# Kernel optimization log

Hardware: AMD Instinct MI355X
Metric: run time of the kernel (lower is better)

The kernel has to match this reference:

```python
import jax, jax.numpy as jnp
import numpy as np

NUM_CODES = 8192
CODE_DEPTH = 64
D_MODEL = 1024
NUM_LEVELS = 1


def setup_inputs() -> dict:
    key = jax.random.key(0)
    k1, k2, k3, k4 = jax.random.split(key, 4)
    x = jax.random.normal(k1, (8, 2048, D_MODEL), dtype=jnp.float32)
    # nn.Linear(d_model, code_depth): weight [code_depth, d_model], bias [code_depth]
    W_down = jax.random.normal(k2, (CODE_DEPTH, D_MODEL), dtype=jnp.float32) * 0.02
    b_down = jnp.zeros((CODE_DEPTH,), dtype=jnp.float32)
    # codebook = torch.randn(num_levels, num_codes, code_depth)
    codebook = jax.random.normal(k3, (NUM_LEVELS, NUM_CODES, CODE_DEPTH), dtype=jnp.float32)
    return {"x": x, "W_down": W_down, "b_down": b_down, "codebook": codebook}


def reference(x, W_down, b_down, codebook):
    # downsample: Linear(d_model -> code_depth), level 0
    soft = jnp.einsum("bsd,cd->bsc", x, W_down) + b_down  # [B,S,C]
    book = codebook[0]  # [K,C]
    # cdist(x, book).argmin == argmin of squared distances (sqrt is monotone)
    x2 = jnp.sum(soft * soft, axis=-1, keepdims=True)      # [B,S,1]
    c2 = jnp.sum(book * book, axis=-1)                     # [K]
    xc = jnp.einsum("bsc,kc->bsk", soft, book)             # [B,S,K]
    sq_dist = x2 - 2.0 * xc + c2                           # [B,S,K]
    code_indices = jnp.argmin(sq_dist, axis=-1)            # [B,S] int
    hard = book[code_indices]                              # [B,S,C]
    # training-mode losses (mse_loss = mean over all elements)
    commitment_loss = jnp.mean((jax.lax.stop_gradient(hard) - soft) ** 2)
    embedding_loss = jnp.mean((hard - jax.lax.stop_gradient(soft)) ** 2)
    # straight-through estimator
    hard_ste = soft + jax.lax.stop_gradient(hard - soft)
    return (soft, code_indices, hard_ste, commitment_loss, embedding_loss)
```

## Files before the change

kernel.cpp:

```cpp
#include <hip/hip_runtime.h>

#define M_TOT   16384
#define DM      1024
#define CD      64
#define NCODES  8192
#define NCHUNK  16
#define CPC     (NCODES / NCHUNK)
#define CTILE   16

#define SOFT_OFF  0
#define IDX_OFF   1048576
#define HARD_OFF  1064960
#define LOSS_OFF  2113536

__global__ __launch_bounds__(256) void compute_c2(const float* __restrict__ book,
                                                  float* __restrict__ c2) {
    const int k = blockIdx.x * 256 + threadIdx.x;
    const float4* p = (const float4*)(book + (size_t)k * CD);
    float s = 0.0f;
#pragma unroll
    for (int q = 0; q < CD / 4; ++q) {
        const float4 v = p[q];
        s = fmaf(v.x, v.x, s);
        s = fmaf(v.y, v.y, s);
        s = fmaf(v.z, v.z, s);
        s = fmaf(v.w, v.w, s);
    }
    c2[k] = s;
}

__global__ __launch_bounds__(1024, 1) void soft_fused(const float* __restrict__ x,
                                                      const float* __restrict__ W,
                                                      const float* __restrict__ bias,
                                                      float* __restrict__ out_soft) {
    __shared__ float smem[8704];
    float (*xt)[16][68] = (float (*)[16][68])smem;
    float (*wt)[16][68] = (float (*)[16][68])(smem + 4352);
    float (*pb)[32][65] = (float (*)[32][65])smem;

    const int tid = threadIdx.x;
    const int kg  = tid >> 8;
    const int t   = tid & 255;
    const int r0  = blockIdx.x * 64;
    const int rg  = t >> 4;
    const int cg  = t & 15;

    float acc[4][4] = {};

    for (int k0 = kg * 256; k0 < kg * 256 + 256; k0 += 16) {
        {
            const int row = t >> 2;
            const int kq  = (t & 3) * 4;
            const float4 v = *(const float4*)(x + (size_t)(r0 + row) * DM + k0 + kq);
            xt[kg][kq + 0][row] = v.x; xt[kg][kq + 1][row] = v.y;
            xt[kg][kq + 2][row] = v.z; xt[kg][kq + 3][row] = v.w;
            const float4 w = *(const float4*)(W + (size_t)row * DM + k0 + kq);
            wt[kg][kq + 0][row] = w.x; wt[kg][kq + 1][row] = w.y;
            wt[kg][kq + 2][row] = w.z; wt[kg][kq + 3][row] = w.w;
        }
        __syncthreads();
#pragma unroll
        for (int kk = 0; kk < 16; ++kk) {
            const float4 xv = *(const float4*)&xt[kg][kk][rg * 4];
            const float4 wv = *(const float4*)&wt[kg][kk][cg * 4];
            const float xa[4] = {xv.x, xv.y, xv.z, xv.w};
            const float wa[4] = {wv.x, wv.y, wv.z, wv.w};
#pragma unroll
            for (int r = 0; r < 4; ++r)
#pragma unroll
                for (int q = 0; q < 4; ++q)
                    acc[r][q] = fmaf(xa[r], wa[q], acc[r][q]);
        }
        __syncthreads();
    }

#pragma unroll
    for (int half = 0; half < 2; ++half) {
        if ((rg >> 3) == half) {
#pragma unroll
            for (int r = 0; r < 4; ++r)
                *(float4*)&pb[kg][(rg & 7) * 4 + r][cg * 4] =
                    make_float4(acc[r][0], acc[r][1], acc[r][2], acc[r][3]);
        }
        __syncthreads();
        if (tid < 512) {
            const int row = tid >> 4;
            const int qd  = tid & 15;
            float4 s = *(const float4*)&pb[0][row][qd * 4];
#pragma unroll
            for (int g = 1; g < 4; ++g) {
                const float4 v = *(const float4*)&pb[g][row][qd * 4];
                s.x += v.x; s.y += v.y; s.z += v.z; s.w += v.w;
            }
            const float4 bb = *(const float4*)(bias + qd * 4);
            s.x += bb.x; s.y += bb.y; s.z += bb.z; s.w += bb.w;
            *(float4*)(out_soft + (size_t)(r0 + half * 32 + row) * CD + qd * 4) = s;
        }
        __syncthreads();
    }
}

__global__ __launch_bounds__(256, 4) void dist_argmin3(const float* __restrict__ soft,
                                                       const float* __restrict__ book,
                                                       const float* __restrict__ c2,
                                                       float* __restrict__ cand_d,
                                                       int* __restrict__ cand_i) {
    const int row   = blockIdx.x * 256 + threadIdx.x;
    const int kbase = blockIdx.y * CPC;
    const float4* sp = (const float4*)(soft + (size_t)row * CD);

    float mind = 3.4e38f;
    int   mini = kbase;

    for (int kt = 0; kt < CPC; kt += CTILE) {
        const float4* bp = (const float4*)(book + (size_t)(kbase + kt) * CD);
        float acc[CTILE] = {};
#pragma unroll
        for (int q = 0; q < 16; ++q) {
            const float4 sv = sp[q];
#pragma unroll
            for (int c = 0; c < CTILE; ++c) {
                const float4 bv = bp[(size_t)c * 16 + q];
                acc[c] = fmaf(sv.x, bv.x, acc[c]);
                acc[c] = fmaf(sv.y, bv.y, acc[c]);
                acc[c] = fmaf(sv.z, bv.z, acc[c]);
                acc[c] = fmaf(sv.w, bv.w, acc[c]);
            }
        }
        const int kk0 = kbase + kt;
#pragma unroll
        for (int c = 0; c < CTILE; ++c) {
            const float dd = fmaf(-2.f, acc[c], c2[kk0 + c]);
            if (dd < mind) { mind = dd; mini = kk0 + c; }
        }
    }

    cand_d[blockIdx.y * M_TOT + row] = mind;
    cand_i[blockIdx.y * M_TOT + row] = mini;
}

__global__ __launch_bounds__(256) void finalize(const float* __restrict__ book,
                                                const float* __restrict__ cand_d,
                                                const int* __restrict__ cand_i,
                                                float* __restrict__ out) {
    __shared__ float rd[256];
    __shared__ int   ri[256];
    __shared__ int   ksels[16];
    __shared__ float red[256];

    const int tid  = threadIdx.x;
    const int rloc = tid >> 4;
    const int g    = tid & 15;
    const int row  = blockIdx.x * 16 + rloc;

    rd[tid] = cand_d[(size_t)g * M_TOT + row];
    ri[tid] = cand_i[(size_t)g * M_TOT + row];
    __syncthreads();

    if (g == 0) {
        float bd = rd[rloc * 16];
        int   bi = ri[rloc * 16];
#pragma unroll
        for (int j = 1; j < 16; ++j) {
            const float dd = rd[rloc * 16 + j];
            if (dd < bd) { bd = dd; bi = ri[rloc * 16 + j]; }
        }
        ksels[rloc] = bi;
        out[IDX_OFF + row] = (float)bi;
    }
    __syncthreads();

    const int k  = ksels[rloc];
    const int dq = g * 4;

    const float4 h = *(const float4*)(book + (size_t)k * CD + dq);
    const float4 s = *(const float4*)(out + SOFT_OFF + (size_t)row * CD + dq);

    const float dx = h.x - s.x, dy = h.y - s.y, dz = h.z - s.z, dw = h.w - s.w;
    float4 ste;
    ste.x = s.x + dx; ste.y = s.y + dy; ste.z = s.z + dz; ste.w = s.w + dw;
    *(float4*)(out + HARD_OFF + (size_t)row * CD + dq) = ste;

    red[tid] = dx * dx + dy * dy + dz * dz + dw * dw;
    __syncthreads();
#pragma unroll
    for (int sh = 128; sh > 0; sh >>= 1) {
        if (tid < sh) red[tid] += red[tid + sh];
        __syncthreads();
    }
    if (tid == 0) {
        const float v = red[0] * (1.0f / (float)(M_TOT * CD));
        atomicAdd(out + LOSS_OFF, v);
        atomicAdd(out + LOSS_OFF + 1, v);
    }
}

extern "C" void kernel_launch(void* const* d_in, const int* in_sizes, int n_in,
                              void* d_out, int out_size, void* d_ws, size_t ws_size,
                              hipStream_t stream) {
    const float* x    = (const float*)d_in[0];
    const float* W    = (const float*)d_in[1];
    const float* bias = (const float*)d_in[2];
    const float* book = (const float*)d_in[3];
    float* out = (float*)d_out;

    float* ws     = (float*)d_ws;
    float* c2     = ws;
    float* cand_d = ws + NCODES;
    int*   cand_i = (int*)(cand_d + NCHUNK * M_TOT);

    compute_c2<<<NCODES / 256, 256, 0, stream>>>(book, c2);
    soft_fused<<<M_TOT / 64, 1024, 0, stream>>>(x, W, bias, out + SOFT_OFF);
    dist_argmin3<<<dim3(M_TOT / 256, NCHUNK), 256, 0, stream>>>(out + SOFT_OFF, book, c2,
                                                                cand_d, cand_i);
    hipMemsetAsync(out + LOSS_OFF, 0, 2 * sizeof(float), stream);
    finalize<<<M_TOT / 16, 256, 0, stream>>>(book, cand_d, cand_i, out);
}
```

Measured before the change: 563.6 us.

## Use bf16 MFMA two-pass distance search with fp32 rescoring of near candidates

Replaces the fp32 scalar distance/argmin kernel with a bf16 MFMA pipeline. A first pass finds each row's approximate minimum distance. A second pass collects every (row, code) pair within a fixed margin of that minimum, and an fp32 rescore picks the exact argmin by 64-bit atomicMin. This moves the dominant 16384x8192x64 GEMM onto matrix cores, at the cost of running the GEMM twice, extra conversion kernels, and atomics. The candidate list is capped and the margin is fixed, so an overflow or a bf16 error larger than the margin could change the selected indices.

```diff
diff --git a/kernel.cpp b/kernel.cpp
--- a/kernel.cpp
+++ b/kernel.cpp
@@ -1,4 +1,5 @@
 #include <hip/hip_runtime.h>
+#include <hip/hip_bf16.h>
 
 #define M_TOT   16384
 #define DM      1024
@@ -7,11 +8,27 @@
 #define NCHUNK  16
 #define CPC     (NCODES / NCHUNK)
 #define CTILE   16
+#define CSPLIT  8
+#define CODES_PER_CHUNK (NCODES / CSPLIT)
+#define DELTA   2.0f
+#define CAP     (1u << 19)
 
 #define SOFT_OFF  0
 #define IDX_OFF   1048576
 #define HARD_OFF  1064960
 #define LOSS_OFF  2113536
+
+typedef __attribute__((ext_vector_type(8)))  short bfrag;
+typedef __attribute__((ext_vector_type(16))) float f32x16;
+
+__device__ __forceinline__ unsigned mapf(float d) {
+    unsigned u = __float_as_uint(d);
+    return (u & 0x80000000u) ? ~u : (u | 0x80000000u);
+}
+__device__ __forceinline__ float unmapf(unsigned m) {
+    unsigned u = (m & 0x80000000u) ? (m ^ 0x80000000u) : ~m;
+    return __uint_as_float(u);
+}
 
 __global__ __launch_bounds__(256) void compute_c2(const float* __restrict__ book,
                                                   float* __restrict__ c2) {
@@ -21,12 +38,25 @@
 #pragma unroll
     for (int q = 0; q < CD / 4; ++q) {
         const float4 v = p[q];
-        s = fmaf(v.x, v.x, s);
-        s = fmaf(v.y, v.y, s);
-        s = fmaf(v.z, v.z, s);
-        s = fmaf(v.w, v.w, s);
+        s = fmaf(v.x, v.x, s); s = fmaf(v.y, v.y, s);
+        s = fmaf(v.z, v.z, s); s = fmaf(v.w, v.w, s);
     }
     c2[k] = s;
+}
+
+__global__ __launch_bounds__(256) void cvt_bf16(const float* __restrict__ src,
+                                                unsigned short* __restrict__ dst,
+                                                int n4) {
+    const int i = blockIdx.x * 256 + threadIdx.x;
+    if (i >= n4) return;
+    const float4 v = ((const float4*)src)[i];
+    ushort4 o;
+    __hip_bfloat16 a;
+    a = __float2bfloat16(v.x); o.x = *(unsigned short*)&a;
+    a = __float2bfloat16(v.y); o.y = *(unsigned short*)&a;
+    a = __float2bfloat16(v.z); o.z = *(unsigned short*)&a;
+    a = __float2bfloat16(v.w); o.w = *(unsigned short*)&a;
+    ((ushort4*)dst)[i] = o;
 }
 
 __global__ __launch_bounds__(1024, 1) void soft_fused(const float* __restrict__ x,
@@ -100,6 +130,163 @@
     }
 }
 
+template<int PASS>
+__global__ __launch_bounds__(256, 4) void mfma_dist(const unsigned short* __restrict__ sbf,
+                                                    const unsigned short* __restrict__ bbf,
+                                                    const float* __restrict__ c2,
+                                                    unsigned* __restrict__ rowmin_u,
+                                                    unsigned* __restrict__ cnt,
+                                                    unsigned* __restrict__ list) {
+    const int tid  = threadIdx.x;
+    const int lane = tid & 63;
+    const int w    = tid >> 6;
+    const int cl   = lane & 31;
+    const int h    = lane >> 5;
+    const int r0w  = blockIdx.x * 128 + w * 32;
+    const int kbase = blockIdx.y * CODES_PER_CHUNK;
+
+    const unsigned short* sp = sbf + (size_t)(r0w + cl) * CD + 8 * h;
+    const bfrag a0 = *(const bfrag*)(sp + 0);
+    const bfrag a1 = *(const bfrag*)(sp + 16);
+    const bfrag a2 = *(const bfrag*)(sp + 32);
+    const bfrag a3 = *(const bfrag*)(sp + 48);
+
+    float rmin[16];
+    float thr[16];
+    if (PASS == 1) {
+#pragma unroll
+        for (int r = 0; r < 16; ++r) rmin[r] = 3.4e38f;
+    } else {
+#pragma unroll
+        for (int r = 0; r < 16; ++r)
+            thr[r] = unmapf(rowmin_u[r0w + (r & 3) + 8 * (r >> 2) + 4 * h]) + DELTA;
+    }
+
+#pragma unroll 2
+    for (int ct = 0; ct < CODES_PER_CHUNK / 32; ++ct) {
+        const int code = kbase + ct * 32 + cl;
+        const unsigned short* bp = bbf + (size_t)code * CD + 8 * h;
+        const bfrag b0 = *(const bfrag*)(bp + 0);
+        const bfrag b1 = *(const bfrag*)(bp + 16);
+        const bfrag b2 = *(const bfrag*)(bp + 32);
+        const bfrag b3 = *(const bfrag*)(bp + 48);
+
+        f32x16 acc;
+#pragma unroll
+        for (int r = 0; r < 16; ++r) acc[r] = 0.0f;
+        acc = __builtin_amdgcn_mfma_f32_32x32x16_bf16(a0, b0, acc, 0, 0, 0);
+        acc = __builtin_amdgcn_mfma_f32_32x32x16_bf16(a1, b1, acc, 0, 0, 0);
+        acc = __builtin_amdgcn_mfma_f32_32x32x16_bf16(a2, b2, acc, 0, 0, 0);
+        acc = __builtin_amdgcn_mfma_f32_32x32x16_bf16(a3, b3, acc, 0, 0, 0);
+
+        const float cc = c2[code];
+        if (PASS == 1) {
+#pragma unroll
+            for (int r = 0; r < 16; ++r)
+                rmin[r] = fminf(rmin[r], fmaf(-2.0f, acc[r], cc));
+        } else {
+            float hitmin = 1.0e30f;
+#pragma unroll
+            for (int r = 0; r < 16; ++r)
+                hitmin = fminf(hitmin, fmaf(-2.0f, acc[r], cc) - thr[r]);
+            if (hitmin < 0.0f) {
+#pragma unroll
+                for (int r = 0; r < 16; ++r) {
+                    const float dist = fmaf(-2.0f, acc[r], cc);
+                    if (dist < thr[r]) {
+                        const unsigned row = r0w + (r & 3) + 8 * (r >> 2) + 4 * h;
+                        const unsigned idx = atomicAdd(cnt, 1u);
+                        if (idx < CAP) list[idx] = (row << 13) | (unsigned)code;
+                    }
+                }
+            }
+        }
+    }
+
+    if (PASS == 1) {
+#pragma unroll
+        for (int r = 0; r < 16; ++r) {
+            float v = rmin[r];
+#pragma unroll
+            for (int m = 1; m <= 16; m <<= 1)
+                v = fminf(v, __shfl_xor(v, m, 64));
+            rmin[r] = v;
+        }
+        if (cl == 0) {
+#pragma unroll
+            for (int r = 0; r < 16; ++r)
+                atomicMin(&rowmin_u[r0w + (r & 3) + 8 * (r >> 2) + 4 * h], mapf(rmin[r]));
+        }
+    }
+}
+
+__global__ __launch_bounds__(256) void rescore(const float* __restrict__ soft,
+                                               const float* __restrict__ book,
+                                               const float* __restrict__ c2,
+                                               const unsigned* __restrict__ cnt,
+                                               const unsigned* __restrict__ list,
+                                               unsigned long long* __restrict__ rowkey) {
+    unsigned n = cnt[0];
+    if (n > CAP) n = CAP;
+    const unsigned i = blockIdx.x * 256 + threadIdx.x;
+    if (i >= n) return;
+    const unsigned pr = list[i];
+    const int row  = pr >> 13;
+    const int code = pr & 8191;
+    const float4* sp = (const float4*)(soft + (size_t)row * CD);
+    const float4* bp = (const float4*)(book + (size_t)code * CD);
+    float a = 0.0f;
+#pragma unroll
+    for (int q = 0; q < 16; ++q) {
+        const float4 s = sp[q], b = bp[q];
+        a = fmaf(s.x, b.x, a); a = fmaf(s.y, b.y, a);
+        a = fmaf(s.z, b.z, a); a = fmaf(s.w, b.w, a);
+    }
+    const float dist = fmaf(-2.0f, a, c2[code]);
+    const unsigned long long key = ((unsigned long long)mapf(dist) << 32) | (unsigned)code;
+    atomicMin(&rowkey[row], key);
+}
+
+__global__ __launch_bounds__(256) void finalize2(const float* __restrict__ book,
+                                                 const unsigned long long* __restrict__ rowkey,
+                                                 float* __restrict__ out) {
+    __shared__ int   ksels[16];
+    __shared__ float red[256];
+    const int tid  = threadIdx.x;
+    const int rloc = tid >> 4;
+    const int g    = tid & 15;
+    const int row  = blockIdx.x * 16 + rloc;
+
+    if (g == 0) {
+        const int k = (int)(unsigned)(rowkey[row] & 0xFFFFFFFFull);
+        ksels[rloc] = k;
+        out[IDX_OFF + row] = (float)k;
+    }
+    __syncthreads();
+
+    const int k  = ksels[rloc];
+    const int dq = g * 4;
+    const float4 h = *(const float4*)(book + (size_t)k * CD + dq);
+    const float4 s = *(const float4*)(out + SOFT_OFF + (size_t)row * CD + dq);
+    const float dx = h.x - s.x, dy = h.y - s.y, dz = h.z - s.z, dw = h.w - s.w;
+    float4 ste;
+    ste.x = s.x + dx; ste.y = s.y + dy; ste.z = s.z + dz; ste.w = s.w + dw;
+    *(float4*)(out + HARD_OFF + (size_t)row * CD + dq) = ste;
+
+    red[tid] = dx * dx + dy * dy + dz * dz + dw * dw;
+    __syncthreads();
+#pragma unroll
+    for (int sh = 128; sh > 0; sh >>= 1) {
+        if (tid < sh) red[tid] += red[tid + sh];
+        __syncthreads();
+    }
+    if (tid == 0) {
+        const float v = red[0] * (1.0f / (float)(M_TOT * CD));
+        atomicAdd(out + LOSS_OFF, v);
+        atomicAdd(out + LOSS_OFF + 1, v);
+    }
+}
+
 __global__ __launch_bounds__(256, 4) void dist_argmin3(const float* __restrict__ soft,
                                                        const float* __restrict__ book,
                                                        const float* __restrict__ c2,
@@ -108,10 +295,8 @@
     const int row   = blockIdx.x * 256 + threadIdx.x;
     const int kbase = blockIdx.y * CPC;
     const float4* sp = (const float4*)(soft + (size_t)row * CD);
-
     float mind = 3.4e38f;
     int   mini = kbase;
-
     for (int kt = 0; kt < CPC; kt += CTILE) {
         const float4* bp = (const float4*)(book + (size_t)(kbase + kt) * CD);
         float acc[CTILE] = {};
@@ -121,10 +306,8 @@
 #pragma unroll
             for (int c = 0; c < CTILE; ++c) {
                 const float4 bv = bp[(size_t)c * 16 + q];
-                acc[c] = fmaf(sv.x, bv.x, acc[c]);
-                acc[c] = fmaf(sv.y, bv.y, acc[c]);
-                acc[c] = fmaf(sv.z, bv.z, acc[c]);
-                acc[c] = fmaf(sv.w, bv.w, acc[c]);
+                acc[c] = fmaf(sv.x, bv.x, acc[c]); acc[c] = fmaf(sv.y, bv.y, acc[c]);
+                acc[c] = fmaf(sv.z, bv.z, acc[c]); acc[c] = fmaf(sv.w, bv.w, acc[c]);
             }
         }
         const int kk0 = kbase + kt;
@@ -134,29 +317,25 @@
             if (dd < mind) { mind = dd; mini = kk0 + c; }
         }
     }
-
     cand_d[blockIdx.y * M_TOT + row] = mind;
     cand_i[blockIdx.y * M_TOT + row] = mini;
 }
 
-__global__ __launch_bounds__(256) void finalize(const float* __restrict__ book,
-                                                const float* __restrict__ cand_d,
-                                                const int* __restrict__ cand_i,
-                                                float* __restrict__ out) {
+__global__ __launch_bounds__(256) void finalize_fb(const float* __restrict__ book,
+                                                   const float* __restrict__ cand_d,
+                                                   const int* __restrict__ cand_i,
+                                                   float* __restrict__ out) {
     __shared__ float rd[256];
     __shared__ int   ri[256];
     __shared__ int   ksels[16];
     __shared__ float red[256];
-
     const int tid  = threadIdx.x;
     const int rloc = tid >> 4;
     const int g    = tid & 15;
     const int row  = blockIdx.x * 16 + rloc;
-
     rd[tid] = cand_d[(size_t)g * M_TOT + row];
     ri[tid] = cand_i[(size_t)g * M_TOT + row];
     __syncthreads();
-
     if (g == 0) {
         float bd = rd[rloc * 16];
         int   bi = ri[rloc * 16];
@@ -169,18 +348,14 @@
         out[IDX_OFF + row] = (float)bi;
     }
     __syncthreads();
-
     const int k  = ksels[rloc];
     const int dq = g * 4;
-
     const float4 h = *(const float4*)(book + (size_t)k * CD + dq);
     const float4 s = *(const float4*)(out + SOFT_OFF + (size_t)row * CD + dq);
-
     const float dx = h.x - s.x, dy = h.y - s.y, dz = h.z - s.z, dw = h.w - s.w;
     float4 ste;
     ste.x = s.x + dx; ste.y = s.y + dy; ste.z = s.z + dz; ste.w = s.w + dw;
     *(float4*)(out + HARD_OFF + (size_t)row * CD + dq) = ste;
-
     red[tid] = dx * dx + dy * dy + dz * dz + dw * dw;
     __syncthreads();
 #pragma unroll
@@ -203,16 +378,44 @@
     const float* bias = (const float*)d_in[2];
     const float* book = (const float*)d_in[3];
     float* out = (float*)d_out;
-
-    float* ws     = (float*)d_ws;
-    float* c2     = ws;
-    float* cand_d = ws + NCODES;
-    int*   cand_i = (int*)(cand_d + NCHUNK * M_TOT);
-
-    compute_c2<<<NCODES / 256, 256, 0, stream>>>(book, c2);
-    soft_fused<<<M_TOT / 64, 1024, 0, stream>>>(x, W, bias, out + SOFT_OFF);
-    dist_argmin3<<<dim3(M_TOT / 256, NCHUNK), 256, 0, stream>>>(out + SOFT_OFF, book, c2,
-                                                                cand_d, cand_i);
+    char* ws = (char*)d_ws;
+
+    unsigned long long* rowkey = (unsigned long long*)(ws);
+    float*    c2       = (float*)(ws + 131072);
+    unsigned* rowmin_u = (unsigned*)(ws + 163840);
+    unsigned* cnt      = (unsigned*)(ws + 229376);
+    unsigned short* soft_bf = (unsigned short*)(ws + 229632);
+    unsigned short* book_bf = (unsigned short*)(ws + 2326784);
+    unsigned* list     = (unsigned*)(ws + 3375360);
+    const size_t NEED  = 5472512;
+
     hipMemsetAsync(out + LOSS_OFF, 0, 2 * sizeof(float), stream);
-    finalize<<<M_TOT / 16, 256, 0, stream>>>(book, cand_d, cand_i, out);
-}
+
+    if (ws_size >= NEED) {
+        compute_c2<<<NCODES / 256, 256, 0, stream>>>(book, c2);
+        cvt_bf16<<<(NCODES * CD / 4 + 255) / 256, 256, 0, stream>>>(book, book_bf,
+                                                                    NCODES * CD / 4);
+        soft_fused<<<M_TOT / 64, 1024, 0, stream>>>(x, W, bias, out + SOFT_OFF);
+        cvt_bf16<<<(M_TOT * CD / 4 + 255) / 256, 256, 0, stream>>>(out + SOFT_OFF, soft_bf,
+                                                                   M_TOT * CD / 4);
+        hipMemsetAsync(rowmin_u, 0xFF, M_TOT * sizeof(unsigned), stream);
+        hipMemsetAsync(rowkey, 0xFF, M_TOT * sizeof(unsigned long long), stream);
+        hipMemsetAsync(cnt, 0, 16, stream);
+
+        mfma_dist<1><<<dim3(M_TOT / 128, CSPLIT), 256, 0, stream>>>(soft_bf, book_bf, c2,
+                                                                    rowmin_u, cnt, list);
+        mfma_dist<2><<<dim3(M_TOT / 128, CSPLIT), 256, 0, stream>>>(soft_bf, book_bf, c2,
+                                                                    rowmin_u, cnt, list);
+        rescore<<<CAP / 256, 256, 0, stream>>>(out + SOFT_OFF, book, c2, cnt, list, rowkey);
+        finalize2<<<M_TOT / 16, 256, 0, stream>>>(book, rowkey, out);
+    } else {
+        float* c2f    = (float*)ws;
+        float* cand_d = c2f + NCODES;
+        int*   cand_i = (int*)(cand_d + NCHUNK * M_TOT);
+        compute_c2<<<NCODES / 256, 256, 0, stream>>>(book, c2f);
+        soft_fused<<<M_TOT / 64, 1024, 0, stream>>>(x, W, bias, out + SOFT_OFF);
+        dist_argmin3<<<dim3(M_TOT / 256, NCHUNK), 256, 0, stream>>>(out + SOFT_OFF, book,
+                                                                    c2f, cand_d, cand_i);
+        finalize_fb<<<M_TOT / 16, 256, 0, stream>>>(book, cand_d, cand_i, out);
+    }
+}
```

Measured after the change: 663.3 us. +17.7%, slower.
